# Optimization experiments

Hardware: AMD Instinct MI355X
Metric: run time of the kernel (lower is better)

## Reference

```python
import jax, jax.numpy as jnp
import numpy as np

CHUNK = 256  # rows of z processed per scan step; keeps [CHUNK, M, D] intermediate ~64MB


def setup_inputs() -> dict:
    key = jax.random.key(0)
    k1, k2, k3, k4 = jax.random.split(key, 4)
    N, M, D = 2048, 512, 128
    z = jax.random.normal(k1, (N, D), dtype=jnp.float32)
    e = jax.random.normal(k2, (M, D), dtype=jnp.float32)
    probs = jax.random.uniform(k3, (N,), dtype=jnp.float32)
    dropout = jax.random.uniform(k4, (N, D), dtype=jnp.float32)
    return {"z": z, "e": e, "probs": probs, "dropout": dropout}


def reference(z, e, probs, dropout):
    # z: [N, D], e: [M, D]
    N, D = z.shape
    M = e.shape[0]
    nchunk = N // CHUNK

    def body(carry, zc):
        # zc: [CHUNK, D]
        min_sum, min_elem = carry  # [M], [M, D]
        # elementwise squared differences for this chunk: [CHUNK, M, D]
        delem = (zc[:, None, :] - e[None, :, :]) ** 2
        dsum = jnp.sum(delem, axis=2)                      # [CHUNK, M]
        min_sum = jnp.minimum(min_sum, jnp.min(dsum, axis=0))
        min_elem = jnp.minimum(min_elem, jnp.min(delem, axis=0))
        return (min_sum, min_elem), None

    init = (jnp.full((M,), jnp.inf, dtype=z.dtype),
            jnp.full((M, D), jnp.inf, dtype=z.dtype))
    (min_sum, min_elem), _ = jax.lax.scan(body, init, z.reshape(nchunk, CHUNK, D))

    # torch: mean over M of min over N of sum_d distance
    min_loss = jnp.mean(min_sum)
    # torch: mean over (M, D) of elementwise min over N
    wise_min_loss = jnp.mean(min_elem)

    # z = z * (dropout < probs[:, None])  -- boolean mask multiply
    z_out = z * (dropout < probs[:, None]).astype(z.dtype)
    return min_loss, wise_min_loss, z_out
```

## Files before the change

kernel.cpp:

```cpp
#include <hip/hip_runtime.h>


#define N_ 2048
#define M_ 512
#define D_ 128
#define PB_SUM  (8 * M_ * D_)
#define ACC_OFF (PB_SUM + M_ * 32)
#define CNT_OFF (ACC_OFF + 2)

__global__ void __launch_bounds__(256, 2) k_main(
        const float* __restrict__ z, const float* __restrict__ e,
        const float* __restrict__ probs, const float* __restrict__ drop,
        float* __restrict__ out, float* __restrict__ ws) {
    const int bx = blockIdx.x;
    const int t  = threadIdx.x;

    if (bx < 512) {
        const int mg = bx >> 3, chunk = bx & 7;
        const int d = t & 127, half = t >> 7;
        const int m0 = mg * 8 + half * 4;
        const int n0 = chunk * 256;

        const float e0 = e[(m0 + 0) * D_ + d];
        const float e1 = e[(m0 + 1) * D_ + d];
        const float e2 = e[(m0 + 2) * D_ + d];
        const float e3 = e[(m0 + 3) * D_ + d];

        float me0 = __uint_as_float(0x7f800000u), me1 = me0, me2 = me0, me3 = me0;
        const float* zp = z + n0 * D_ + d;
        #pragma unroll 8
        for (int i = 0; i < 256; ++i) {
            float zv = zp[i * D_];
            float df;
            df = zv - e0; me0 = fminf(me0, df * df);
            df = zv - e1; me1 = fminf(me1, df * df);
            df = zv - e2; me2 = fminf(me2, df * df);
            df = zv - e3; me3 = fminf(me3, df * df);
        }
        float* pe = ws + (size_t)chunk * (M_ * D_) + m0 * D_ + d;
        pe[0 * D_] = me0;
        pe[1 * D_] = me1;
        pe[2 * D_] = me2;
        pe[3 * D_] = me3;
    } else if (bx < 768) {
        const int b = bx - 512;
        const int nb = b >> 5, mt = b & 31;
        const int n = nb * 256 + t;
        const int m0 = mt * 16;

        float4 zr[32];
        const float4* z4 = reinterpret_cast<const float4*>(z) + n * 32;
        #pragma unroll
        for (int j = 0; j < 32; ++j) zr[j] = z4[j];

        const float4* e4 = reinterpret_cast<const float4*>(e);
        const int w = t >> 6;
        for (int mi = 0; mi < 16; mi += 2) {
            const int ma = m0 + mi;
            const int mb = ma + 1;
            float a0 = 0.f, a1 = 0.f, a2 = 0.f, a3 = 0.f;
            float b0 = 0.f, b1 = 0.f, b2 = 0.f, b3 = 0.f;
            #pragma unroll
            for (int j = 0; j < 32; ++j) {
                float4 ea = e4[ma * 32 + j];
                float4 eb = e4[mb * 32 + j];
                float dx, dy, dz, dw;
                dx = zr[j].x - ea.x; a0 = fmaf(dx, dx, a0);
                dy = zr[j].y - ea.y; a1 = fmaf(dy, dy, a1);
                dz = zr[j].z - ea.z; a2 = fmaf(dz, dz, a2);
                dw = zr[j].w - ea.w; a3 = fmaf(dw, dw, a3);
                dx = zr[j].x - eb.x; b0 = fmaf(dx, dx, b0);
                dy = zr[j].y - eb.y; b1 = fmaf(dy, dy, b1);
                dz = zr[j].z - eb.z; b2 = fmaf(dz, dz, b2);
                dw = zr[j].w - eb.w; b3 = fmaf(dw, dw, b3);
            }
            float sa = (a0 + a1) + (a2 + a3);
            float sb = (b0 + b1) + (b2 + b3);
            #pragma unroll
            for (int off = 32; off; off >>= 1) {
                sa = fminf(sa, __shfl_xor(sa, off));
                sb = fminf(sb, __shfl_xor(sb, off));
            }
            if ((t & 63) == 0) {
                ws[PB_SUM + ma * 32 + nb * 4 + w] = sa;
                ws[PB_SUM + mb * 32 + nb * 4 + w] = sb;
            }
        }
    } else {
        const int b = bx - 768;
        const int i = b * 256 + t;
        const int n = i >> 5;
        const float p = probs[n];
        const float4 zv = reinterpret_cast<const float4*>(z)[i];
        const float4 dv = reinterpret_cast<const float4*>(drop)[i];
        float2 lo, hi;
        lo.x = dv.x < p ? zv.x : 0.f;
        lo.y = dv.y < p ? zv.y : 0.f;
        hi.x = dv.z < p ? zv.z : 0.f;
        hi.y = dv.w < p ? zv.w : 0.f;
        float2* o = reinterpret_cast<float2*>(out + 2) + i * 2;
        o[0] = lo;
        o[1] = hi;
        if (b == 0 && t == 0) {
            ws[ACC_OFF] = 0.f;
            ws[ACC_OFF + 1] = 0.f;
            reinterpret_cast<unsigned int*>(ws)[CNT_OFF] = 0u;
        }
    }
}

__device__ __forceinline__ float min4(float4 v) {
    return fminf(fminf(v.x, v.y), fminf(v.z, v.w));
}

__global__ void __launch_bounds__(256) k_fin(float* __restrict__ ws,
                                             float* __restrict__ out) {
    const int b = blockIdx.x, t = threadIdx.x;
    float* acc = ws + ACC_OFF;
    unsigned int* cnt = reinterpret_cast<unsigned int*>(ws) + CNT_OFF;

    const int cell = b * 1024 + t * 4;
    float4 mv = *reinterpret_cast<const float4*>(ws + cell);
    #pragma unroll
    for (int c = 1; c < 8; ++c) {
        float4 v = *reinterpret_cast<const float4*>(ws + c * (M_ * D_) + cell);
        mv.x = fminf(mv.x, v.x); mv.y = fminf(mv.y, v.y);
        mv.z = fminf(mv.z, v.z); mv.w = fminf(mv.w, v.w);
    }
    float s_elem = (mv.x + mv.y) + (mv.z + mv.w);

    float s_sum = 0.f;
    if (t < 64) {
        const int m = b * 8 + (t >> 3);
        const int j = t & 7;
        float4 v = *reinterpret_cast<const float4*>(ws + PB_SUM + m * 32 + j * 4);
        float mn = min4(v);
        mn = fminf(mn, __shfl_xor(mn, 1));
        mn = fminf(mn, __shfl_xor(mn, 2));
        mn = fminf(mn, __shfl_xor(mn, 4));
        if ((t & 7) == 0) s_sum = mn;
    }

    #pragma unroll
    for (int off = 32; off; off >>= 1) {
        s_elem += __shfl_xor(s_elem, off);
        s_sum  += __shfl_xor(s_sum, off);
    }
    __shared__ float sm[8];
    const int w = t >> 6;
    if ((t & 63) == 0) { sm[w] = s_elem; sm[4 + w] = s_sum; }
    __syncthreads();
    if (t == 0) {
        float te = sm[0] + sm[1] + sm[2] + sm[3];
        float ts = sm[4] + sm[5] + sm[6] + sm[7];
        atomicAdd(&acc[0], ts);
        atomicAdd(&acc[1], te);
        __threadfence();
        unsigned int old = atomicAdd(cnt, 1u);
        if (old == 63u) {
            float a0 = atomicAdd(&acc[0], 0.f);
            float a1 = atomicAdd(&acc[1], 0.f);
            out[0] = a0 * (1.0f / 512.0f);
            out[1] = a1 * (1.0f / 65536.0f);
        }
    }
}

extern "C" void kernel_launch(void* const* d_in, const int* in_sizes, int n_in,
                              void* d_out, int out_size, void* d_ws, size_t ws_size,
                              hipStream_t stream) {
    const float* z     = (const float*)d_in[0];
    const float* e     = (const float*)d_in[1];
    const float* probs = (const float*)d_in[2];
    const float* drop  = (const float*)d_in[3];
    float* out = (float*)d_out;
    float* ws  = (float*)d_ws;

    k_main<<<dim3(1024), dim3(256), 0, stream>>>(z, e, probs, drop, out, ws);
    k_fin<<<dim3(64), dim3(256), 0, stream>>>(ws, out);
}
```

Measured before the change: 87.50 us.

## Raise per-thread m reuse and chunk z registers to cut register pressure

The elementwise-min blocks now handle 8 codebook rows per thread instead of 4, halving their block count and reusing each z load across more rows. The distance-sum blocks no longer hold a full 128-float z row in registers. They process D in four chunks of 32 and keep 16 running sums, doing the min-shuffle reduction once at the end. Launch bounds rise to 4 blocks per CU, which targets higher occupancy. The trade-off is fewer blocks overall (768), which may underfill the GPU, and more accumulators per thread.

```diff
diff --git a/kernel.cpp b/kernel.cpp
--- a/kernel.cpp
+++ b/kernel.cpp
@@ -8,86 +8,85 @@
 #define ACC_OFF (PB_SUM + M_ * 32)
 #define CNT_OFF (ACC_OFF + 2)
 
-__global__ void __launch_bounds__(256, 2) k_main(
+__global__ void __launch_bounds__(256, 4) k_main(
         const float* __restrict__ z, const float* __restrict__ e,
         const float* __restrict__ probs, const float* __restrict__ drop,
         float* __restrict__ out, float* __restrict__ ws) {
     const int bx = blockIdx.x;
     const int t  = threadIdx.x;
 
-    if (bx < 512) {
+    if (bx < 256) {
         const int mg = bx >> 3, chunk = bx & 7;
         const int d = t & 127, half = t >> 7;
-        const int m0 = mg * 8 + half * 4;
+        const int m0 = mg * 16 + half * 8;
         const int n0 = chunk * 256;
 
-        const float e0 = e[(m0 + 0) * D_ + d];
-        const float e1 = e[(m0 + 1) * D_ + d];
-        const float e2 = e[(m0 + 2) * D_ + d];
-        const float e3 = e[(m0 + 3) * D_ + d];
-
-        float me0 = __uint_as_float(0x7f800000u), me1 = me0, me2 = me0, me3 = me0;
+        float ev[8], mn[8];
+        #pragma unroll
+        for (int k = 0; k < 8; ++k) {
+            ev[k] = e[(m0 + k) * D_ + d];
+            mn[k] = __uint_as_float(0x7f800000u);
+        }
         const float* zp = z + n0 * D_ + d;
         #pragma unroll 8
         for (int i = 0; i < 256; ++i) {
             float zv = zp[i * D_];
-            float df;
-            df = zv - e0; me0 = fminf(me0, df * df);
-            df = zv - e1; me1 = fminf(me1, df * df);
-            df = zv - e2; me2 = fminf(me2, df * df);
-            df = zv - e3; me3 = fminf(me3, df * df);
+            #pragma unroll
+            for (int k = 0; k < 8; ++k) {
+                float df = zv - ev[k];
+                mn[k] = fminf(mn[k], df * df);
+            }
         }
         float* pe = ws + (size_t)chunk * (M_ * D_) + m0 * D_ + d;
-        pe[0 * D_] = me0;
-        pe[1 * D_] = me1;
-        pe[2 * D_] = me2;
-        pe[3 * D_] = me3;
-    } else if (bx < 768) {
-        const int b = bx - 512;
+        #pragma unroll
+        for (int k = 0; k < 8; ++k) pe[k * D_] = mn[k];
+    } else if (bx < 512) {
+        const int b = bx - 256;
         const int nb = b >> 5, mt = b & 31;
         const int n = nb * 256 + t;
         const int m0 = mt * 16;
 
-        float4 zr[32];
+        float s[16];
+        #pragma unroll
+        for (int k = 0; k < 16; ++k) s[k] = 0.f;
+
         const float4* z4 = reinterpret_cast<const float4*>(z) + n * 32;
-        #pragma unroll
-        for (int j = 0; j < 32; ++j) zr[j] = z4[j];
+        const float4* e4 = reinterpret_cast<const float4*>(e);
 
-        const float4* e4 = reinterpret_cast<const float4*>(e);
-        const int w = t >> 6;
-        for (int mi = 0; mi < 16; mi += 2) {
-            const int ma = m0 + mi;
-            const int mb = ma + 1;
-            float a0 = 0.f, a1 = 0.f, a2 = 0.f, a3 = 0.f;
-            float b0 = 0.f, b1 = 0.f, b2 = 0.f, b3 = 0.f;
+        #pragma unroll 1
+        for (int dc = 0; dc < 4; ++dc) {
+            float4 zq[8];
             #pragma unroll
-            for (int j = 0; j < 32; ++j) {
-                float4 ea = e4[ma * 32 + j];
-                float4 eb = e4[mb * 32 + j];
-                float dx, dy, dz, dw;
-                dx = zr[j].x - ea.x; a0 = fmaf(dx, dx, a0);
-                dy = zr[j].y - ea.y; a1 = fmaf(dy, dy, a1);
-                dz = zr[j].z - ea.z; a2 = fmaf(dz, dz, a2);
-                dw = zr[j].w - ea.w; a3 = fmaf(dw, dw, a3);
-                dx = zr[j].x - eb.x; b0 = fmaf(dx, dx, b0);
-                dy = zr[j].y - eb.y; b1 = fmaf(dy, dy, b1);
-                dz = zr[j].z - eb.z; b2 = fmaf(dz, dz, b2);
-                dw = zr[j].w - eb.w; b3 = fmaf(dw, dw, b3);
-            }
-            float sa = (a0 + a1) + (a2 + a3);
-            float sb = (b0 + b1) + (b2 + b3);
+            for (int jj = 0; jj < 8; ++jj) zq[jj] = z4[dc * 8 + jj];
             #pragma unroll
-            for (int off = 32; off; off >>= 1) {
-                sa = fminf(sa, __shfl_xor(sa, off));
-                sb = fminf(sb, __shfl_xor(sb, off));
-            }
-            if ((t & 63) == 0) {
-                ws[PB_SUM + ma * 32 + nb * 4 + w] = sa;
-                ws[PB_SUM + mb * 32 + nb * 4 + w] = sb;
+            for (int k = 0; k < 16; ++k) {
+                const float4* ep = e4 + (m0 + k) * 32 + dc * 8;
+                float a0 = 0.f, a1 = 0.f, a2 = 0.f, a3 = 0.f;
+                #pragma unroll
+                for (int jj = 0; jj < 8; ++jj) {
+                    float4 evq = ep[jj];
+                    float dx = zq[jj].x - evq.x; a0 = fmaf(dx, dx, a0);
+                    float dy = zq[jj].y - evq.y; a1 = fmaf(dy, dy, a1);
+                    float dz = zq[jj].z - evq.z; a2 = fmaf(dz, dz, a2);
+                    float dw = zq[jj].w - evq.w; a3 = fmaf(dw, dw, a3);
+                }
+                s[k] += (a0 + a1) + (a2 + a3);
             }
         }
+        #pragma unroll
+        for (int off = 32; off; off >>= 1) {
+            #pragma unroll
+            for (int k = 0; k < 16; ++k)
+                s[k] = fminf(s[k], __shfl_xor(s[k], off));
+        }
+        if ((t & 63) == 0) {
+            const int w = t >> 6;
+            #pragma unroll
+            for (int k = 0; k < 16; ++k)
+                ws[PB_SUM + (m0 + k) * 32 + nb * 4 + w] = s[k];
+        }
     } else {
-        const int b = bx - 768;
+        const int b = bx - 512;
         const int i = b * 256 + t;
         const int n = i >> 5;
         const float p = probs[n];
@@ -176,6 +175,6 @@
     float* out = (float*)d_out;
     float* ws  = (float*)d_ws;
 
-    k_main<<<dim3(1024), dim3(256), 0, stream>>>(z, e, probs, drop, out, ws);
+    k_main<<<dim3(768), dim3(256), 0, stream>>>(z, e, probs, drop, out, ws);
     k_fin<<<dim3(64), dim3(256), 0, stream>>>(ws, out);
 }
```

New measurement: 91.24 us. 4.3% more time.
